# Performance work log

Hardware: AMD Instinct MI355X
Metric: run time of the kernel (lower is better)

Reference implementation:

```python
import jax, jax.numpy as jnp
import numpy as np

BETA = 0.25  # commitment loss weight


def setup_inputs() -> dict:
    key = jax.random.key(0)
    k1, k2 = jax.random.split(key)
    B, D, H, W = 16, 256, 64, 64
    K = 2048  # num_codebook
    z = jax.random.normal(k1, (B, D, H, W), dtype=jnp.float32)
    # matches nn.Embedding init uniform_(-1/K, 1/K) in scale-free way; values irrelevant to math
    codebook = jax.random.uniform(k2, (K, D), dtype=jnp.float32,
                                  minval=-1.0 / K, maxval=1.0 / K)
    return {"z": z, "codebook": codebook}


def reference(z, codebook):
    # z: (B, D, H, W) -> (B, H, W, D) -> (N, D)
    b, d, h, w = z.shape
    k = codebook.shape[0]
    z_flat = jnp.transpose(z, (0, 2, 3, 1)).reshape(-1, d)  # (N, D)

    # squared L2 distance via sum-of-squares + matmul (same expansion as torch code)
    distance = (jnp.sum(z_flat * z_flat, axis=1, keepdims=True)
                + jnp.sum(codebook * codebook, axis=1)
                - 2.0 * jnp.matmul(z_flat, codebook.T))  # (N, K)
    vq_indices = jnp.argmin(distance, axis=1)  # (N,)
    z_quantized = codebook[vq_indices]  # (N, D) gather

    # one-hot counting (scatter-add, equivalent to sum of one-hot)
    vq_current_count = jnp.zeros((k,), dtype=jnp.int32).at[vq_indices].add(1)

    sg = jax.lax.stop_gradient
    codebook_loss = jnp.mean((z_quantized - sg(z_flat)) ** 2)
    commitment_loss = jnp.mean((z_flat - sg(z_quantized)) ** 2)
    loss = codebook_loss + BETA * commitment_loss

    # straight-through estimator
    z_st = z_flat + sg(z_quantized - z_flat)
    q = jnp.transpose(z_st.reshape(b, h, w, d), (0, 3, 1, 2))  # (B, D, H, W)
    return q, loss, codebook_loss, commitment_loss, vq_current_count
```

## Files before the change

### kernel.cpp

```cpp
#include <hip/hip_runtime.h>

#define N_TOT 65536
#define K_CB  2048
#define D_DIM 256
#define HW    4096
#define DHW   1048576

typedef _Float16 half8 __attribute__((ext_vector_type(8)));
typedef _Float16 half4v __attribute__((ext_vector_type(4)));
typedef float f32x16 __attribute__((ext_vector_type(16)));


__device__ __forceinline__ void gload_lds16(const void* g, void* l) {
    __builtin_amdgcn_global_load_lds((const __attribute__((address_space(1))) void*)g,
                                     (__attribute__((address_space(3))) void*)l, 16, 0, 0);
}

__device__ __forceinline__ float pw128_sq(const float* __restrict__ base, int stride) {
    #pragma clang fp contract(off)
    float r[8];
    #pragma unroll
    for (int j = 0; j < 8; ++j) { float v = base[j * stride]; r[j] = v * v; }
    for (int i = 8; i < 128; i += 8) {
        #pragma unroll
        for (int j = 0; j < 8; ++j) { float v = base[(i + j) * stride]; r[j] += v * v; }
    }
    return ((r[0] + r[1]) + (r[2] + r[3])) + ((r[4] + r[5]) + (r[6] + r[7]));
}

__global__ void cbnorm_zero_kernel(const float* __restrict__ cb, float* __restrict__ cb2,
                                   int* __restrict__ counts, float* __restrict__ sse) {
    #pragma clang fp contract(off)
    int k = blockIdx.x * 256 + threadIdx.x;
    const float* row = cb + (size_t)k * D_DIM;
    cb2[k] = pw128_sq(row, 1) + pw128_sq(row + 128, 1);
    counts[k] = 0;
    if (k == 0) *sse = 0.f;
}

__global__ void split_c_kernel(const float* __restrict__ cb,
                               _Float16* __restrict__ ch, _Float16* __restrict__ cl) {
    int e = (blockIdx.x * 256 + threadIdx.x) * 4;
    float4 v = *(const float4*)(cb + e);
    float xs[4] = {v.x, v.y, v.z, v.w};
    half4v hh, hl;
    #pragma unroll
    for (int u = 0; u < 4; ++u) {
        float x = xs[u] * 16384.0f;
        _Float16 hv = (_Float16)x;
        hh[u] = hv;
        hl[u] = (_Float16)(x - (float)hv);
    }
    *(half4v*)(ch + e) = hh;
    *(half4v*)(cl + e) = hl;
}

__global__ void fused_z_kernel(const float* __restrict__ z,
                               _Float16* __restrict__ zh, _Float16* __restrict__ zl,
                               float* __restrict__ z2,
                               unsigned long long* __restrict__ rowmin_g) {
    __shared__ __align__(16) float lt[256 * 33];
    __shared__ float rj[512];
    __shared__ float hh[64];
    int t = threadIdx.x;
    int n0 = blockIdx.x * 32;
    int b = n0 >> 12, s0 = n0 & 4095;
    const float* zb = z + (size_t)b * DHW + s0;

    #pragma unroll
    for (int v = 0; v < 8; ++v) {
        int f = v * 256 + t;
        int d = f >> 3, nch = f & 7;
        float4 val = *(const float4*)(zb + (size_t)d * HW + nch * 4);
        lt[d * 33 + nch * 4 + 0] = val.x;
        lt[d * 33 + nch * 4 + 1] = val.y;
        lt[d * 33 + nch * 4 + 2] = val.z;
        lt[d * 33 + nch * 4 + 3] = val.w;
    }
    __syncthreads();

    {
        #pragma clang fp contract(off)
        int n = t & 31, j = t >> 5;
        #pragma unroll
        for (int hf = 0; hf < 2; ++hf) {
            float r = 0.f;
            #pragma unroll
            for (int i = 0; i < 16; ++i) {
                float v = lt[(hf * 128 + i * 8 + j) * 33 + n];
                r += v * v;
            }
            rj[n * 16 + hf * 8 + j] = r;
        }
    }

    #pragma unroll
    for (int v = 0; v < 8; ++v) {
        int g = v * 256 + t;
        int n = g >> 6, du = g & 63;
        half4v hv, lv;
        #pragma unroll
        for (int u = 0; u < 4; ++u) {
            float x = lt[(du * 4 + u) * 33 + n] * 2048.0f;
            _Float16 h = (_Float16)x;
            hv[u] = h;
            lv[u] = (_Float16)(x - (float)h);
        }
        size_t off = (size_t)(n0 + n) * 256 + du * 4;
        *(half4v*)(zh + off) = hv;
        *(half4v*)(zl + off) = lv;
    }
    __syncthreads();

    if (t < 64) {
        #pragma clang fp contract(off)
        int n = t & 31, hf = t >> 5;
        const float* r = &rj[n * 16 + hf * 8];
        hh[hf * 32 + n] = ((r[0] + r[1]) + (r[2] + r[3])) + ((r[4] + r[5]) + (r[6] + r[7]));
    }
    __syncthreads();
    if (t < 32) {
        #pragma clang fp contract(off)
        z2[n0 + t] = hh[t] + hh[32 + t];
        rowmin_g[n0 + t] = ~0ull;
    }
}

__launch_bounds__(256, 2)
__global__ void argmin_mfma_kernel(const _Float16* __restrict__ zh, const _Float16* __restrict__ zl,
                                   const _Float16* __restrict__ ch, const _Float16* __restrict__ cl,
                                   const float* __restrict__ cb2, const float* __restrict__ z2arr,
                                   unsigned long long* __restrict__ rowmin_g) {
    __shared__ __align__(16) char lds_raw[49152];
    _Float16* lds_a = (_Float16*)lds_raw;
    _Float16* lds_b = (_Float16*)(lds_raw + 16384);

    int t = threadIdx.x;
    int r0 = (blockIdx.x >> 3) * 128;
    int c0 = (blockIdx.x & 7) * 256;
    int w = t >> 6, lane = t & 63;
    int wi = w & 1, wj = w >> 1;
    int l31 = lane & 31, l5 = lane >> 5;

    f32x16 acc[2][4];
    #pragma unroll
    for (int i = 0; i < 2; ++i)
        #pragma unroll
        for (int j = 0; j < 4; ++j)
            #pragma unroll
            for (int r = 0; r < 16; ++r) acc[i][j][r] = 0.f;

    float c2v[4];
    #pragma unroll
    for (int j = 0; j < 4; ++j)
        c2v[j] = cb2[c0 + wj * 128 + j * 32 + l31];

    for (int ki = 0; ki < 12; ++ki) {
        int seg  = ki >> 2;
        int koff = (ki & 3) * 64;
        const _Float16* asrc = (seg < 2) ? zh : zl;
        const _Float16* bsrc = (seg == 1) ? cl : ch;
        __syncthreads();
        #pragma unroll
        for (int v = 0; v < 4; ++v) {
            int p = v * 256 + t;
            int row = p >> 3;
            int ku = (p & 7) ^ (row & 7);
            gload_lds16(asrc + (size_t)(r0 + row) * 256 + koff + ku * 8, lds_a + p * 8);
        }
        #pragma unroll
        for (int v = 0; v < 8; ++v) {
            int p = v * 256 + t;
            int row = p >> 3;
            int ku = (p & 7) ^ (row & 7);
            gload_lds16(bsrc + (size_t)(c0 + row) * 256 + koff + ku * 8, lds_b + p * 8);
        }
        __syncthreads();
        #pragma unroll
        for (int ks = 0; ks < 4; ++ks) {
            half8 af[2], bf[4];
            #pragma unroll
            for (int i = 0; i < 2; ++i) {
                int row = wi * 64 + i * 32 + l31;
                int ku  = (ks * 2 + l5) ^ (row & 7);
                af[i] = *(half8*)(lds_a + row * 64 + ku * 8);
            }
            #pragma unroll
            for (int j = 0; j < 4; ++j) {
                int row = wj * 128 + j * 32 + l31;
                int ku  = (ks * 2 + l5) ^ (row & 7);
                bf[j] = *(half8*)(lds_b + row * 64 + ku * 8);
            }
            #pragma unroll
            for (int i = 0; i < 2; ++i)
                #pragma unroll
                for (int j = 0; j < 4; ++j)
                    acc[i][j] = __builtin_amdgcn_mfma_f32_32x32x16_f16(af[i], bf[j], acc[i][j], 0, 0, 0);
        }
    }

    __syncthreads();
    unsigned long long* scratch = (unsigned long long*)lds_raw;
    #pragma unroll
    for (int i = 0; i < 2; ++i) {
        #pragma unroll
        for (int rg = 0; rg < 16; ++rg) {
            int rowoff = (rg & 3) + 8 * (rg >> 2) + 4 * l5;
            int m = wi * 64 + i * 32 + rowoff;
            float zz = z2arr[r0 + m];
            unsigned long long key = ~0ull;
            #pragma unroll
            for (int j = 0; j < 4; ++j) {
                float sc = (zz + c2v[j]) - acc[i][j][rg] * (1.0f / 16777216.0f);
                unsigned long long k2 = ((unsigned long long)__float_as_uint(sc) << 32)
                                      | (unsigned)(c0 + wj * 128 + j * 32 + l31);
                key = (k2 < key) ? k2 : key;
            }
            {
                unsigned lo = (unsigned)key, hi = (unsigned)(key >> 32);
                unsigned olo = __shfl_xor(lo, 16);
                unsigned ohi = __shfl_xor(hi, 16);
                unsigned long long o = ((unsigned long long)ohi << 32) | olo;
                key = (o < key) ? o : key;
            }
            if (l31 < 16) scratch[m * 34 + wj * 16 + l31] = key;
        }
    }
    __syncthreads();
    if (t < 128) {
        const ulonglong2* srow = (const ulonglong2*)(scratch + t * 34);
        unsigned long long best = ~0ull;
        #pragma unroll
        for (int s = 0; s < 16; ++s) {
            ulonglong2 p = srow[s];
            if (p.x < best) best = p.x;
            if (p.y < best) best = p.y;
        }
        atomicMin(&rowmin_g[r0 + t], best);
    }
}

__global__ void gather_kernel(const float* __restrict__ z, const float* __restrict__ cb,
                              const unsigned long long* __restrict__ rowmin_g,
                              float* __restrict__ qout,
                              float* __restrict__ sse, int* __restrict__ counts) {
    int t = threadIdx.x;
    int si = t & 63, dg = t >> 6;
    int n = blockIdx.x * 64 + si;
    int idx = (int)(rowmin_g[n] & 0xFFFFFFFFull);
    int b = n >> 12, s = n & 4095;
    const float* zb = z + (size_t)b * DHW + s;
    float*       qb = qout + (size_t)b * DHW + s;
    const float4* crow = (const float4*)(cb + (size_t)idx * D_DIM + dg * 64);
    float acc = 0.f;
    #pragma unroll
    for (int dd4 = 0; dd4 < 16; ++dd4) {
        float4 q4 = crow[dd4];
        float qv[4] = {q4.x, q4.y, q4.z, q4.w};
        #pragma unroll
        for (int u = 0; u < 4; ++u) {
            int d = dg * 64 + dd4 * 4 + u;
            float zv = zb[(size_t)d * HW];
            qb[(size_t)d * HW] = qv[u];
            float df = zv - qv[u];
            acc += df * df;
        }
    }
    #pragma unroll
    for (int off = 32; off > 0; off >>= 1) acc += __shfl_down(acc, off, 64);
    if ((t & 63) == 0) atomicAdd(sse, acc);
    if (dg == 0) atomicAdd(&counts[idx], 1);
}

__global__ void finalize_kernel(const float* __restrict__ sse, const int* __restrict__ counts,
                                float* __restrict__ out) {
    int t = threadIdx.x;
    float mse = *sse * (1.0f / 16777216.0f);
    if (t == 0) {
        out[16777216] = mse * 1.25f;
        out[16777217] = mse;
        out[16777218] = mse;
    }
    for (int i = t; i < 2048; i += 256) out[16777219 + i] = (float)counts[i];
}

extern "C" void kernel_launch(void* const* d_in, const int* in_sizes, int n_in,
                              void* d_out, int out_size, void* d_ws, size_t ws_size,
                              hipStream_t stream) {
    const float* z  = (const float*)d_in[0];
    const float* cb = (const float*)d_in[1];
    float* out = (float*)d_out;
    float* ws  = (float*)d_ws;

    float* cb2    = ws;
    int*   counts = (int*)(ws + 2048);
    float* sse    = ws + 4096;
    float* z2     = ws + 4352;
    unsigned long long* rowmin_g = (unsigned long long*)(ws + 69888);
    _Float16* ch  = (_Float16*)(ws + 200960);
    _Float16* cl  = (_Float16*)(ws + 463104);

    _Float16* zzh = (_Float16*)d_out;
    _Float16* zzl = zzh + 16777216;

    cbnorm_zero_kernel<<<8, 256, 0, stream>>>(cb, cb2, counts, sse);
    split_c_kernel<<<512, 256, 0, stream>>>(cb, ch, cl);
    fused_z_kernel<<<2048, 256, 0, stream>>>(z, zzh, zzl, z2, rowmin_g);
    argmin_mfma_kernel<<<4096, 256, 0, stream>>>(zzh, zzl, ch, cl, cb2, z2, rowmin_g);
    gather_kernel<<<1024, 256, 0, stream>>>(z, cb, rowmin_g, out, sse, counts);
    finalize_kernel<<<1, 256, 0, stream>>>(sse, counts, out);
}
```

Measured before the change: 462.3 us.

## Double-buffer LDS staging with 256x256 tiles and 512-thread argmin blocks

The MFMA argmin kernel moves from a single-buffered 128x256 tile on 256 threads to a double-buffered 256x256 tile on 512 threads (128 KB of LDS). Global-to-LDS loads for the next K-slice are issued while the current slice is being computed, which is meant to hide load latency and cut the per-slice barrier stalls. The larger tile raises data reuse per loaded byte. A block-index swizzle changes the order in which tiles are visited, and the epilogue gains an extra cross-lane shuffle reduction. The trade-off is that the large LDS footprint limits each CU to one block and raises register pressure, so occupancy drops.

New measurement: 488.5 us. 1.06x slower.

```diff
diff --git a/kernel.cpp b/kernel.cpp
--- a/kernel.cpp
+++ b/kernel.cpp
@@ -126,108 +126,134 @@
     }
 }
 
-__launch_bounds__(256, 2)
+
+__device__ __forceinline__ void stage_tile(int ki,
+        const _Float16* __restrict__ zh, const _Float16* __restrict__ zl,
+        const _Float16* __restrict__ ch, const _Float16* __restrict__ cl,
+        int r0, int c0, int t, _Float16* la, _Float16* lb) {
+    int seg  = ki >> 2;
+    int koff = (ki & 3) * 64;
+    const _Float16* asrc = (seg < 2) ? zh : zl;
+    const _Float16* bsrc = (seg == 1) ? cl : ch;
+    #pragma unroll
+    for (int v = 0; v < 4; ++v) {
+        int p = v * 512 + t;
+        int row = p >> 3;
+        int ku = (p & 7) ^ (row & 7);
+        gload_lds16(asrc + (size_t)(r0 + row) * 256 + koff + ku * 8, la + (size_t)p * 8);
+    }
+    #pragma unroll
+    for (int v = 0; v < 4; ++v) {
+        int p = v * 512 + t;
+        int row = p >> 3;
+        int ku = (p & 7) ^ (row & 7);
+        gload_lds16(bsrc + (size_t)(c0 + row) * 256 + koff + ku * 8, lb + (size_t)p * 8);
+    }
+}
+
+__device__ __forceinline__ void compute_tile(const _Float16* la, const _Float16* lb,
+        int wm, int wn, int l31, int l5, f32x16 acc[4][2]) {
+    #pragma unroll
+    for (int ks = 0; ks < 4; ++ks) {
+        half8 af[4], bf[2];
+        #pragma unroll
+        for (int i = 0; i < 4; ++i) {
+            int row = wm * 128 + i * 32 + l31;
+            int ku  = (ks * 2 + l5) ^ (row & 7);
+            af[i] = *(const half8*)(la + row * 64 + ku * 8);
+        }
+        #pragma unroll
+        for (int j = 0; j < 2; ++j) {
+            int row = wn * 64 + j * 32 + l31;
+            int ku  = (ks * 2 + l5) ^ (row & 7);
+            bf[j] = *(const half8*)(lb + row * 64 + ku * 8);
+        }
+        #pragma unroll
+        for (int i = 0; i < 4; ++i)
+            #pragma unroll
+            for (int j = 0; j < 2; ++j)
+                acc[i][j] = __builtin_amdgcn_mfma_f32_32x32x16_f16(af[i], bf[j], acc[i][j], 0, 0, 0);
+    }
+}
+
+__device__ __forceinline__ unsigned long long kmin_xor(unsigned long long key, int m) {
+    unsigned lo = (unsigned)key, hi = (unsigned)(key >> 32);
+    unsigned olo = __shfl_xor(lo, m);
+    unsigned ohi = __shfl_xor(hi, m);
+    unsigned long long o = ((unsigned long long)ohi << 32) | olo;
+    return (o < key) ? o : key;
+}
+
+__launch_bounds__(512, 2)
 __global__ void argmin_mfma_kernel(const _Float16* __restrict__ zh, const _Float16* __restrict__ zl,
                                    const _Float16* __restrict__ ch, const _Float16* __restrict__ cl,
                                    const float* __restrict__ cb2, const float* __restrict__ z2arr,
                                    unsigned long long* __restrict__ rowmin_g) {
-    __shared__ __align__(16) char lds_raw[49152];
-    _Float16* lds_a = (_Float16*)lds_raw;
-    _Float16* lds_b = (_Float16*)(lds_raw + 16384);
+    __shared__ __align__(16) char lds_raw[131072];
+    _Float16* a0 = (_Float16*)lds_raw;
+    _Float16* b0 = (_Float16*)(lds_raw + 32768);
+    _Float16* a1 = (_Float16*)(lds_raw + 65536);
+    _Float16* b1 = (_Float16*)(lds_raw + 98304);
 
     int t = threadIdx.x;
-    int r0 = (blockIdx.x >> 3) * 128;
-    int c0 = (blockIdx.x & 7) * 256;
+    int bid = blockIdx.x;
+    int swz = (bid & 7) * 256 + (bid >> 3);
+    int r0 = (swz >> 3) * 256;
+    int c0 = (swz & 7) * 256;
     int w = t >> 6, lane = t & 63;
-    int wi = w & 1, wj = w >> 1;
+    int wm = w >> 2, wn = w & 3;
     int l31 = lane & 31, l5 = lane >> 5;
 
-    f32x16 acc[2][4];
-    #pragma unroll
-    for (int i = 0; i < 2; ++i)
-        #pragma unroll
-        for (int j = 0; j < 4; ++j)
+    f32x16 acc[4][2];
+    #pragma unroll
+    for (int i = 0; i < 4; ++i)
+        #pragma unroll
+        for (int j = 0; j < 2; ++j)
             #pragma unroll
             for (int r = 0; r < 16; ++r) acc[i][j][r] = 0.f;
 
-    float c2v[4];
-    #pragma unroll
-    for (int j = 0; j < 4; ++j)
-        c2v[j] = cb2[c0 + wj * 128 + j * 32 + l31];
-
-    for (int ki = 0; ki < 12; ++ki) {
-        int seg  = ki >> 2;
-        int koff = (ki & 3) * 64;
-        const _Float16* asrc = (seg < 2) ? zh : zl;
-        const _Float16* bsrc = (seg == 1) ? cl : ch;
+    float c2v[2];
+    #pragma unroll
+    for (int j = 0; j < 2; ++j)
+        c2v[j] = cb2[c0 + wn * 64 + j * 32 + l31];
+
+    stage_tile(0, zh, zl, ch, cl, r0, c0, t, a0, b0);
+    __syncthreads();
+
+    #pragma unroll 1
+    for (int kp = 0; kp < 6; ++kp) {
+        stage_tile(kp * 2 + 1, zh, zl, ch, cl, r0, c0, t, a1, b1);
+        compute_tile(a0, b0, wm, wn, l31, l5, acc);
         __syncthreads();
-        #pragma unroll
-        for (int v = 0; v < 4; ++v) {
-            int p = v * 256 + t;
-            int row = p >> 3;
-            int ku = (p & 7) ^ (row & 7);
-            gload_lds16(asrc + (size_t)(r0 + row) * 256 + koff + ku * 8, lds_a + p * 8);
-        }
-        #pragma unroll
-        for (int v = 0; v < 8; ++v) {
-            int p = v * 256 + t;
-            int row = p >> 3;
-            int ku = (p & 7) ^ (row & 7);
-            gload_lds16(bsrc + (size_t)(c0 + row) * 256 + koff + ku * 8, lds_b + p * 8);
-        }
+        if (kp < 5)
+            stage_tile(kp * 2 + 2, zh, zl, ch, cl, r0, c0, t, a0, b0);
+        compute_tile(a1, b1, wm, wn, l31, l5, acc);
         __syncthreads();
-        #pragma unroll
-        for (int ks = 0; ks < 4; ++ks) {
-            half8 af[2], bf[4];
-            #pragma unroll
-            for (int i = 0; i < 2; ++i) {
-                int row = wi * 64 + i * 32 + l31;
-                int ku  = (ks * 2 + l5) ^ (row & 7);
-                af[i] = *(half8*)(lds_a + row * 64 + ku * 8);
-            }
-            #pragma unroll
-            for (int j = 0; j < 4; ++j) {
-                int row = wj * 128 + j * 32 + l31;
-                int ku  = (ks * 2 + l5) ^ (row & 7);
-                bf[j] = *(half8*)(lds_b + row * 64 + ku * 8);
-            }
-            #pragma unroll
-            for (int i = 0; i < 2; ++i)
-                #pragma unroll
-                for (int j = 0; j < 4; ++j)
-                    acc[i][j] = __builtin_amdgcn_mfma_f32_32x32x16_f16(af[i], bf[j], acc[i][j], 0, 0, 0);
-        }
-    }
-
-    __syncthreads();
+    }
+
     unsigned long long* scratch = (unsigned long long*)lds_raw;
     #pragma unroll
-    for (int i = 0; i < 2; ++i) {
+    for (int i = 0; i < 4; ++i) {
         #pragma unroll
         for (int rg = 0; rg < 16; ++rg) {
             int rowoff = (rg & 3) + 8 * (rg >> 2) + 4 * l5;
-            int m = wi * 64 + i * 32 + rowoff;
+            int m = wm * 128 + i * 32 + rowoff;
             float zz = z2arr[r0 + m];
             unsigned long long key = ~0ull;
             #pragma unroll
-            for (int j = 0; j < 4; ++j) {
+            for (int j = 0; j < 2; ++j) {
                 float sc = (zz + c2v[j]) - acc[i][j][rg] * (1.0f / 16777216.0f);
                 unsigned long long k2 = ((unsigned long long)__float_as_uint(sc) << 32)
-                                      | (unsigned)(c0 + wj * 128 + j * 32 + l31);
+                                      | (unsigned)(c0 + wn * 64 + j * 32 + l31);
                 key = (k2 < key) ? k2 : key;
             }
-            {
-                unsigned lo = (unsigned)key, hi = (unsigned)(key >> 32);
-                unsigned olo = __shfl_xor(lo, 16);
-                unsigned ohi = __shfl_xor(hi, 16);
-                unsigned long long o = ((unsigned long long)ohi << 32) | olo;
-                key = (o < key) ? o : key;
-            }
-            if (l31 < 16) scratch[m * 34 + wj * 16 + l31] = key;
-        }
-    }
-    __syncthreads();
-    if (t < 128) {
+            key = kmin_xor(key, 16);
+            key = kmin_xor(key, 8);
+            if (l31 < 8) scratch[m * 34 + wn * 8 + l31] = key;
+        }
+    }
+    __syncthreads();
+    if (t < 256) {
         const ulonglong2* srow = (const ulonglong2*)(scratch + t * 34);
         unsigned long long best = ~0ull;
         #pragma unroll
@@ -306,7 +332,7 @@
     cbnorm_zero_kernel<<<8, 256, 0, stream>>>(cb, cb2, counts, sse);
     split_c_kernel<<<512, 256, 0, stream>>>(cb, ch, cl);
     fused_z_kernel<<<2048, 256, 0, stream>>>(z, zzh, zzl, z2, rowmin_g);
-    argmin_mfma_kernel<<<4096, 256, 0, stream>>>(zzh, zzl, ch, cl, cb2, z2, rowmin_g);
+    argmin_mfma_kernel<<<2048, 512, 0, stream>>>(zzh, zzl, ch, cl, cb2, z2, rowmin_g);
     gather_kernel<<<1024, 256, 0, stream>>>(z, cb, rowmin_g, out, sse, counts);
     finalize_kernel<<<1, 256, 0, stream>>>(sse, counts, out);
 }
```

## Shrink argmin GEMM tile to 128x128 with higher occupancy and block swizzle

Applied to the files above, without the earlier changes.

The argmin MFMA kernel tile drops from 128x256 to 128x128 codebook columns per block, halving accumulators, B-tile loads and LDS per block. Launch bounds go up to 4 blocks per CU and the grid doubles to 8192. A blockIdx swizzle is added so concurrently scheduled blocks share z row tiles, with the argmin reduction adjusted to the new layout. The aim is more waves to hide memory latency, at the cost of lower arithmetic intensity per loaded byte and more atomicMin traffic.

New measurement: 453.9 us. About the same (-1.8%).

```diff
diff --git a/kernel.cpp b/kernel.cpp
--- a/kernel.cpp
+++ b/kernel.cpp
@@ -126,34 +126,45 @@
     }
 }
 
-__launch_bounds__(256, 2)
+
+__device__ __forceinline__ unsigned long long kmin_xor(unsigned long long key, int m) {
+    unsigned lo = (unsigned)key, hi = (unsigned)(key >> 32);
+    unsigned olo = __shfl_xor(lo, m);
+    unsigned ohi = __shfl_xor(hi, m);
+    unsigned long long o = ((unsigned long long)ohi << 32) | olo;
+    return (o < key) ? o : key;
+}
+
+__launch_bounds__(256, 4)
 __global__ void argmin_mfma_kernel(const _Float16* __restrict__ zh, const _Float16* __restrict__ zl,
                                    const _Float16* __restrict__ ch, const _Float16* __restrict__ cl,
                                    const float* __restrict__ cb2, const float* __restrict__ z2arr,
                                    unsigned long long* __restrict__ rowmin_g) {
-    __shared__ __align__(16) char lds_raw[49152];
+    __shared__ __align__(16) char lds_raw[32768];
     _Float16* lds_a = (_Float16*)lds_raw;
     _Float16* lds_b = (_Float16*)(lds_raw + 16384);
 
     int t = threadIdx.x;
-    int r0 = (blockIdx.x >> 3) * 128;
-    int c0 = (blockIdx.x & 7) * 256;
+    int bid = blockIdx.x;
+    int swz = (bid & 7) * 1024 + (bid >> 3);
+    int r0 = (swz >> 4) * 128;
+    int c0 = (swz & 15) * 128;
     int w = t >> 6, lane = t & 63;
-    int wi = w & 1, wj = w >> 1;
+    int wm = w >> 1, wn = w & 1;
     int l31 = lane & 31, l5 = lane >> 5;
 
-    f32x16 acc[2][4];
+    f32x16 acc[2][2];
     #pragma unroll
     for (int i = 0; i < 2; ++i)
         #pragma unroll
-        for (int j = 0; j < 4; ++j)
+        for (int j = 0; j < 2; ++j)
             #pragma unroll
             for (int r = 0; r < 16; ++r) acc[i][j][r] = 0.f;
 
-    float c2v[4];
-    #pragma unroll
-    for (int j = 0; j < 4; ++j)
-        c2v[j] = cb2[c0 + wj * 128 + j * 32 + l31];
+    float c2v[2];
+    #pragma unroll
+    for (int j = 0; j < 2; ++j)
+        c2v[j] = cb2[c0 + wn * 64 + j * 32 + l31];
 
     for (int ki = 0; ki < 12; ++ki) {
         int seg  = ki >> 2;
@@ -166,72 +177,67 @@
             int p = v * 256 + t;
             int row = p >> 3;
             int ku = (p & 7) ^ (row & 7);
-            gload_lds16(asrc + (size_t)(r0 + row) * 256 + koff + ku * 8, lds_a + p * 8);
-        }
-        #pragma unroll
-        for (int v = 0; v < 8; ++v) {
+            gload_lds16(asrc + (size_t)((r0 + row) * 256 + koff + ku * 8), lds_a + p * 8);
+        }
+        #pragma unroll
+        for (int v = 0; v < 4; ++v) {
             int p = v * 256 + t;
             int row = p >> 3;
             int ku = (p & 7) ^ (row & 7);
-            gload_lds16(bsrc + (size_t)(c0 + row) * 256 + koff + ku * 8, lds_b + p * 8);
+            gload_lds16(bsrc + (size_t)((c0 + row) * 256 + koff + ku * 8), lds_b + p * 8);
         }
         __syncthreads();
         #pragma unroll
         for (int ks = 0; ks < 4; ++ks) {
-            half8 af[2], bf[4];
+            half8 af[2], bf[2];
             #pragma unroll
             for (int i = 0; i < 2; ++i) {
-                int row = wi * 64 + i * 32 + l31;
+                int row = wm * 64 + i * 32 + l31;
                 int ku  = (ks * 2 + l5) ^ (row & 7);
-                af[i] = *(half8*)(lds_a + row * 64 + ku * 8);
+                af[i] = *(const half8*)(lds_a + row * 64 + ku * 8);
             }
             #pragma unroll
-            for (int j = 0; j < 4; ++j) {
-                int row = wj * 128 + j * 32 + l31;
+            for (int j = 0; j < 2; ++j) {
+                int row = wn * 64 + j * 32 + l31;
                 int ku  = (ks * 2 + l5) ^ (row & 7);
-                bf[j] = *(half8*)(lds_b + row * 64 + ku * 8);
+                bf[j] = *(const half8*)(lds_b + row * 64 + ku * 8);
             }
             #pragma unroll
             for (int i = 0; i < 2; ++i)
                 #pragma unroll
-                for (int j = 0; j < 4; ++j)
+                for (int j = 0; j < 2; ++j)
                     acc[i][j] = __builtin_amdgcn_mfma_f32_32x32x16_f16(af[i], bf[j], acc[i][j], 0, 0, 0);
         }
     }
-
-    __syncthreads();
+    __syncthreads();
+
     unsigned long long* scratch = (unsigned long long*)lds_raw;
     #pragma unroll
     for (int i = 0; i < 2; ++i) {
         #pragma unroll
         for (int rg = 0; rg < 16; ++rg) {
             int rowoff = (rg & 3) + 8 * (rg >> 2) + 4 * l5;
-            int m = wi * 64 + i * 32 + rowoff;
+            int m = wm * 64 + i * 32 + rowoff;
             float zz = z2arr[r0 + m];
             unsigned long long key = ~0ull;
             #pragma unroll
-            for (int j = 0; j < 4; ++j) {
+            for (int j = 0; j < 2; ++j) {
                 float sc = (zz + c2v[j]) - acc[i][j][rg] * (1.0f / 16777216.0f);
                 unsigned long long k2 = ((unsigned long long)__float_as_uint(sc) << 32)
-                                      | (unsigned)(c0 + wj * 128 + j * 32 + l31);
+                                      | (unsigned)(c0 + wn * 64 + j * 32 + l31);
                 key = (k2 < key) ? k2 : key;
             }
-            {
-                unsigned lo = (unsigned)key, hi = (unsigned)(key >> 32);
-                unsigned olo = __shfl_xor(lo, 16);
-                unsigned ohi = __shfl_xor(hi, 16);
-                unsigned long long o = ((unsigned long long)ohi << 32) | olo;
-                key = (o < key) ? o : key;
-            }
-            if (l31 < 16) scratch[m * 34 + wj * 16 + l31] = key;
+            key = kmin_xor(key, 16);
+            key = kmin_xor(key, 8);
+            if (l31 < 8) scratch[m * 18 + wn * 8 + l31] = key;
         }
     }
     __syncthreads();
     if (t < 128) {
-        const ulonglong2* srow = (const ulonglong2*)(scratch + t * 34);
+        const ulonglong2* srow = (const ulonglong2*)(scratch + t * 18);
         unsigned long long best = ~0ull;
         #pragma unroll
-        for (int s = 0; s < 16; ++s) {
+        for (int s = 0; s < 8; ++s) {
             ulonglong2 p = srow[s];
             if (p.x < best) best = p.x;
             if (p.y < best) best = p.y;
@@ -306,7 +312,7 @@
     cbnorm_zero_kernel<<<8, 256, 0, stream>>>(cb, cb2, counts, sse);
     split_c_kernel<<<512, 256, 0, stream>>>(cb, ch, cl);
     fused_z_kernel<<<2048, 256, 0, stream>>>(z, zzh, zzl, z2, rowmin_g);
-    argmin_mfma_kernel<<<4096, 256, 0, stream>>>(zzh, zzl, ch, cl, cb2, z2, rowmin_g);
+    argmin_mfma_kernel<<<8192, 256, 0, stream>>>(zzh, zzl, ch, cl, cb2, z2, rowmin_g);
     gather_kernel<<<1024, 256, 0, stream>>>(z, cb, rowmin_g, out, sse, counts);
     finalize_kernel<<<1, 256, 0, stream>>>(sse, counts, out);
 }
```
